# Kernel tuning notes

Hardware: AMD Instinct MI355X
Metric: run time of the kernel (lower is better)

Reference implementation:

```python
import jax, jax.numpy as jnp
import numpy as np
import math

N_QUBITS = 8
N_QLAYERS = 1
LN_EPS = 1e-5


def _rx(state, theta, wire, n):
    # state: (N, 2,...,2) complex64 with n qubit axes; theta: (N,)
    sh = (theta.shape[0],) + (1,) * (n - 1)
    c = jnp.cos(theta / 2).reshape(sh)
    s = jnp.sin(theta / 2).reshape(sh)
    a = jax.lax.index_in_dim(state, 0, wire + 1, keepdims=False)
    b = jax.lax.index_in_dim(state, 1, wire + 1, keepdims=False)
    return jnp.stack([c * a - 1j * s * b, -1j * s * a + c * b], axis=wire + 1)


def _cnot(state, cw, tw, n):
    s0 = jax.lax.index_in_dim(state, 0, cw + 1, keepdims=False)
    s1 = jax.lax.index_in_dim(state, 1, cw + 1, keepdims=False)
    t_ax = tw + 1 if tw < cw else tw  # target axis index after removing control axis
    s1 = jnp.flip(s1, axis=t_ax)
    return jnp.stack([s0, s1], axis=cw + 1)


def _quantum(angles, qweights):
    # AngleEmbedding (RX) + BasicEntanglerLayers (RX + CNOT ring) + PauliZ expvals
    # angles: (N, 8) float; qweights: (1, 8) float -> returns (N, 8) float
    n = N_QUBITS
    N = angles.shape[0]
    state = jnp.zeros((N,) + (2,) * n, jnp.complex64)
    state = state.at[(slice(None),) + (0,) * n].set(1.0 + 0j)
    for w in range(n):
        state = _rx(state, angles[:, w], w, n)
    for l in range(N_QLAYERS):
        for w in range(n):
            state = _rx(state, jnp.broadcast_to(qweights[l, w], (N,)), w, n)
        for cw in range(n):
            state = _cnot(state, cw, (cw + 1) % n, n)
    probs = state.real ** 2 + state.imag ** 2
    zs = []
    for w in range(n):
        p = probs.sum(axis=tuple(a for a in range(1, n + 1) if a != w + 1))  # (N, 2)
        zs.append(p[:, 0] - p[:, 1])
    return jnp.stack(zs, axis=-1)


def _layernorm(x, g, b):
    m = x.mean(-1, keepdims=True)
    v = ((x - m) ** 2).mean(-1, keepdims=True)
    return (x - m) / jnp.sqrt(v + LN_EPS) * g + b


def _forward(x, Wq, Wk, Wv, Wo, ln1_g, ln1_b, W1, b1, W2, b2, ln2_g, ln2_b,
             ql1_w, ql1_b, qweights, ql2_w, ql2_b):
    B, S, D = x.shape
    H = 16
    dk = D // H
    q = (x @ Wq.T).reshape(B, S, H, dk)
    k = (x @ Wk.T).reshape(B, S, H, dk)
    v = (x @ Wv.T).reshape(B, S, H, dk)
    scores = jnp.einsum('bqhd,bkhd->bhqk', q, k) * (1.0 / math.sqrt(dk))
    attn = jax.nn.softmax(scores, axis=-1)
    o = jnp.einsum('bhqk,bkhd->bqhd', attn, v).reshape(B, S, D) @ Wo.T
    x = _layernorm(o + x, ln1_g, ln1_b)
    ff = jax.nn.relu(x @ W1.T + b1) @ W2.T + b2
    x = _layernorm(ff + x, ln2_g, ln2_b)
    angles = (x @ ql1_w.T + ql1_b).reshape(B * S, N_QUBITS)
    z = _quantum(angles, qweights).reshape(B, S, N_QUBITS).astype(x.dtype)
    y = jnp.concatenate([z, x], axis=2) @ ql2_w.T + ql2_b
    return y


def setup_inputs() -> dict:
    key = jax.random.key(0)
    ks = jax.random.split(key, 12)
    B, S, D, F = 4, 1024, 1024, 4096
    sc = 0.02
    w = lambda k, *sh: jax.random.normal(k, sh, jnp.float32) * sc
    return {
        'x': jax.random.normal(ks[0], (B, S, D), jnp.float32),
        'Wq': w(ks[1], D, D), 'Wk': w(ks[2], D, D), 'Wv': w(ks[3], D, D), 'Wo': w(ks[4], D, D),
        'ln1_g': jnp.ones((D,), jnp.float32), 'ln1_b': jnp.zeros((D,), jnp.float32),
        'W1': w(ks[5], F, D), 'b1': jnp.zeros((F,), jnp.float32),
        'W2': w(ks[6], D, F), 'b2': jnp.zeros((D,), jnp.float32),
        'ln2_g': jnp.ones((D,), jnp.float32), 'ln2_b': jnp.zeros((D,), jnp.float32),
        'ql1_w': w(ks[7], N_QUBITS, D), 'ql1_b': jnp.zeros((N_QUBITS,), jnp.float32),
        'qweights': jax.random.uniform(ks[8], (N_QLAYERS, N_QUBITS), jnp.float32, 0.0, 2 * np.pi),
        'ql2_w': w(ks[9], D, D + N_QUBITS), 'ql2_b': jnp.zeros((D,), jnp.float32),
    }


def reference(x, Wq, Wk, Wv, Wo, ln1_g, ln1_b, W1, b1, W2, b2, ln2_g, ln2_b,
              ql1_w, ql1_b, qweights, ql2_w, ql2_b):
    return _forward(x, Wq, Wk, Wv, Wo, ln1_g, ln1_b, W1, b1, W2, b2, ln2_g, ln2_b,
                    ql1_w, ql1_b, qweights, ql2_w, ql2_b)
```

## Files before the change

kernel.cpp:

```cpp
#include <hip/hip_runtime.h>
#include <hip/hip_bf16.h>

typedef __bf16 bf16_t;
typedef __attribute__((ext_vector_type(8))) __bf16 bf16x8;
typedef __attribute__((ext_vector_type(4))) float floatx4;

#define BM 128

enum { EPI_NONE = 0, EPI_RESID, EPI_BIAS_RELU, EPI_BIAS_RESID, EPI_QL2, EPI_PART };

__device__ __forceinline__ void gld_lds16(const bf16_t* g, bf16_t* l) {
  __builtin_amdgcn_global_load_lds(
      (__attribute__((address_space(1))) void*)(g),
      (__attribute__((address_space(3))) void*)(l), 16, 0, 0);
}

template<int ROWS, int COLS>
__device__ __forceinline__ void stage_swz(const bf16_t* g, int ld, bf16_t* lds, int tid) {
  constexpr int G = COLS / 8;
  #pragma unroll
  for (int i = 0; i < ROWS * G / 256; ++i) {
    int ci = i * 256 + tid;
    int row = ci / G, cc = ci % G;
    int gg = (G == 8) ? (cc ^ (row & 7)) : ((cc & 8) | ((cc & 7) ^ (row & 7)));
    gld_lds16(g + (size_t)row * ld + gg * 8, lds + ci * 8);
  }
}

__device__ __forceinline__ int xcd_remap(int id, int nwg) {
  return (id & 7) * (nwg >> 3) + (id >> 3);
}

__device__ __forceinline__ void core128(const bf16_t* __restrict__ Ag,
                                        const bf16_t* __restrict__ Bg,
                                        int Kloop, int lda, int ldb,
                                        bf16_t* As, bf16_t* Bs,
                                        floatx4 acc[4][4]) {
  const int tid = threadIdx.x;
  const int wid = tid >> 6, lane = tid & 63;
  const int wm = (wid >> 1) * 64, wn = (wid & 1) * 64;
  const int m16 = lane & 15, quad = lane >> 4;
  const int r7 = m16 & 7;
  constexpr int BUF = BM * 64;
  stage_swz<128, 64>(Ag, lda, As, tid);
  stage_swz<128, 64>(Bg, ldb, Bs, tid);
  asm volatile("s_waitcnt vmcnt(0)" ::: "memory");
  __syncthreads();
  int cur = 0;
  for (int k0 = 0; k0 < Kloop; k0 += 64) {
    if (k0 + 64 < Kloop) {
      stage_swz<128, 64>(Ag + k0 + 64, lda, As + (cur ^ 1) * BUF, tid);
      stage_swz<128, 64>(Bg + k0 + 64, ldb, Bs + (cur ^ 1) * BUF, tid);
    }
    const bf16_t* Ab = As + cur * BUF;
    const bf16_t* Bb = Bs + cur * BUF;
    #pragma unroll
    for (int ks = 0; ks < 2; ++ks) {
      const int gi = ks * 4 + quad;
      const int slot = gi ^ r7;
      bf16x8 af[4], bfr[4];
      #pragma unroll
      for (int mt = 0; mt < 4; ++mt)
        af[mt] = *(const bf16x8*)&Ab[((wm + mt * 16 + m16) * 8 + slot) * 8];
      #pragma unroll
      for (int nt = 0; nt < 4; ++nt)
        bfr[nt] = *(const bf16x8*)&Bb[((wn + nt * 16 + m16) * 8 + slot) * 8];
      #pragma unroll
      for (int mt = 0; mt < 4; ++mt)
        #pragma unroll
        for (int nt = 0; nt < 4; ++nt)
          acc[mt][nt] = __builtin_amdgcn_mfma_f32_16x16x32_bf16(af[mt], bfr[nt], acc[mt][nt], 0, 0, 0);
    }
    asm volatile("s_waitcnt vmcnt(0)" ::: "memory");
    __syncthreads();
    cur ^= 1;
  }
}

template<int EPI>
__global__ __launch_bounds__(256)
void gemm128(const bf16_t* __restrict__ A, const bf16_t* __restrict__ B,
             bf16_t* __restrict__ C, const float* __restrict__ bias,
             int N, int K, int mblocks, int nblocks) {
  __shared__ bf16_t As[2 * BM * 64];
  __shared__ bf16_t Bs[2 * BM * 64];
  const int tid = threadIdx.x;
  const int wid = tid >> 6, lane = tid & 63;
  const int wm = (wid >> 1) * 64, wn = (wid & 1) * 64;
  const int m16 = lane & 15, quad = lane >> 4;
  const int id = xcd_remap(blockIdx.x, gridDim.x);
  const int per_group = 8 * nblocks;
  const int grp = id / per_group, rem = id % per_group;
  const int m0 = (grp * 8 + (rem & 7)) * BM;
  const int n0 = (rem >> 3) * BM;
  floatx4 acc[4][4];
  const floatx4 vzero = {0.f, 0.f, 0.f, 0.f};
  #pragma unroll
  for (int mt = 0; mt < 4; ++mt)
    #pragma unroll
    for (int nt = 0; nt < 4; ++nt) acc[mt][nt] = vzero;
  core128(A + (size_t)m0 * K, B + (size_t)n0 * K, K, K, K, As, Bs, acc);
  #pragma unroll
  for (int mt = 0; mt < 4; ++mt)
    #pragma unroll
    for (int nt = 0; nt < 4; ++nt) {
      const int gcol = n0 + wn + nt * 16 + m16;
      float bv = (EPI == EPI_BIAS_RELU) ? bias[gcol] : 0.f;
      #pragma unroll
      for (int r = 0; r < 4; ++r) {
        const int grow = m0 + wm + mt * 16 + quad * 4 + r;
        float v = acc[mt][nt][r];
        if (EPI == EPI_BIAS_RELU) { v += bv; v = fmaxf(v, 0.f); }
        C[(size_t)grow * N + gcol] = (bf16_t)v;
      }
    }
}

__global__ __launch_bounds__(256)
void gemm128_sk(const bf16_t* __restrict__ A, const bf16_t* __restrict__ B,
                bf16_t* __restrict__ p0, bf16_t* __restrict__ p1,
                int N, int K, int ldb, int mblocks, int nblocks) {
  __shared__ bf16_t As[2 * BM * 64];
  __shared__ bf16_t Bs[2 * BM * 64];
  const int tid = threadIdx.x;
  const int wid = tid >> 6, lane = tid & 63;
  const int wm = (wid >> 1) * 64, wn = (wid & 1) * 64;
  const int m16 = lane & 15, quad = lane >> 4;
  const int id = xcd_remap(blockIdx.x, gridDim.x);
  const int per_kh = mblocks * nblocks;
  const int kh = id / per_kh;
  const int rem2 = id % per_kh;
  const int per_group = 8 * nblocks;
  const int grp = rem2 / per_group, rem = rem2 % per_group;
  const int m0 = (grp * 8 + (rem & 7)) * BM;
  const int n0 = (rem >> 3) * BM;
  const int Keff = K / 2;
  floatx4 acc[4][4];
  const floatx4 vzero = {0.f, 0.f, 0.f, 0.f};
  #pragma unroll
  for (int mt = 0; mt < 4; ++mt)
    #pragma unroll
    for (int nt = 0; nt < 4; ++nt) acc[mt][nt] = vzero;
  core128(A + (size_t)m0 * K + (size_t)kh * Keff,
          B + (size_t)n0 * ldb + (size_t)kh * Keff, Keff, K, ldb, As, Bs, acc);
  bf16_t* Cp = kh ? p1 : p0;
  #pragma unroll
  for (int mt = 0; mt < 4; ++mt)
    #pragma unroll
    for (int nt = 0; nt < 4; ++nt) {
      const int gcol = n0 + wn + nt * 16 + m16;
      #pragma unroll
      for (int r = 0; r < 4; ++r) {
        const int grow = m0 + wm + mt * 16 + quad * 4 + r;
        Cp[(size_t)grow * N + gcol] = (bf16_t)acc[mt][nt][r];
      }
    }
}

__global__ __launch_bounds__(256)
void gemm_qkv(const bf16_t* __restrict__ X, const bf16_t* __restrict__ Wb,
              bf16_t* __restrict__ Qo, bf16_t* __restrict__ Ko, bf16_t* __restrict__ Vt) {
  __shared__ bf16_t As[2 * BM * 64];
  __shared__ bf16_t Bs[2 * BM * 64];
  const int tid = threadIdx.x;
  const int wid = tid >> 6, lane = tid & 63;
  const int wm = (wid >> 1) * 64, wn = (wid & 1) * 64;
  const int m16 = lane & 15, quad = lane >> 4;
  const int id = xcd_remap(blockIdx.x, gridDim.x);
  const int per_group = 8 * 24;
  const int grp = id / per_group, rem = id % per_group;
  const int m0 = (grp * 8 + (rem & 7)) * BM;
  const int nall = rem >> 3;
  const int n0 = (nall & 7) * BM;
  const int sel = nall >> 3;
  const bf16_t* B = Wb + (size_t)sel * 1024 * 1024;
  floatx4 acc[4][4];
  const floatx4 vzero = {0.f, 0.f, 0.f, 0.f};
  #pragma unroll
  for (int mt = 0; mt < 4; ++mt)
    #pragma unroll
    for (int nt = 0; nt < 4; ++nt) acc[mt][nt] = vzero;
  core128(X + (size_t)m0 * 1024, B + (size_t)n0 * 1024, 1024, 1024, 1024, As, Bs, acc);
  if (sel < 2) {
    bf16_t* C = sel ? Ko : Qo;
    const float sc = sel ? 1.f : 0.125f;
    #pragma unroll
    for (int mt = 0; mt < 4; ++mt)
      #pragma unroll
      for (int nt = 0; nt < 4; ++nt) {
        const int gcol = n0 + wn + nt * 16 + m16;
        #pragma unroll
        for (int r = 0; r < 4; ++r) {
          const int grow = m0 + wm + mt * 16 + quad * 4 + r;
          C[(size_t)grow * 1024 + gcol] = (bf16_t)(acc[mt][nt][r] * sc);
        }
      }
  } else {
    #pragma unroll
    for (int mt = 0; mt < 4; ++mt) {
      const int grow0 = m0 + wm + mt * 16 + quad * 4;
      const int b = grow0 >> 10, s = grow0 & 1023;
      #pragma unroll
      for (int nt = 0; nt < 4; ++nt) {
        const int gcol = n0 + wn + nt * 16 + m16;
        const int h = gcol >> 6, d = gcol & 63;
        #pragma unroll
        for (int r = 0; r < 4; ++r)
          Vt[(((size_t)b * 16 + h) * 64 + d) * 1024 + s + r] = (bf16_t)acc[mt][nt][r];
      }
    }
  }
}

template<int EPI, bool OUTF32>
__global__ __launch_bounds__(256)
void gemm64(const bf16_t* __restrict__ A, const bf16_t* __restrict__ B,
            void* __restrict__ Cv,
            const bf16_t* __restrict__ resid, const float* __restrict__ bias,
            const bf16_t* __restrict__ z, const float* __restrict__ zw,
            int N, int K, int ldb, int boff, int mblocks) {
  __shared__ bf16_t As[BM * 128];
  __shared__ bf16_t Bs[64 * 128];
  const int tid = threadIdx.x;
  const int wid = tid >> 6, lane = tid & 63;
  const int wm = (wid >> 1) * 64, wn = (wid & 1) * 32;
  const int m16 = lane & 15, quad = lane >> 4;
  const int r7 = m16 & 7;
  const int id = xcd_remap(blockIdx.x, gridDim.x);
  const int nb_ = N >> 6;
  const int per_group = 8 * nb_;
  const int grp = id / per_group, rem = id % per_group;
  const int m0 = (grp * 8 + (rem & 7)) * BM;
  const int n0 = (rem >> 3) * 64;
  const bf16_t* Ag = A + (size_t)m0 * K;
  const bf16_t* Bg = B + (size_t)n0 * ldb + boff;
  floatx4 acc[4][2];
  const floatx4 vzero = {0.f, 0.f, 0.f, 0.f};
  #pragma unroll
  for (int mt = 0; mt < 4; ++mt)
    #pragma unroll
    for (int nt = 0; nt < 2; ++nt) acc[mt][nt] = vzero;
  for (int k0 = 0; k0 < K; k0 += 128) {
    stage_swz<128, 128>(Ag + k0, K, As, tid);
    stage_swz<64, 128>(Bg + k0, ldb, Bs, tid);
    __syncthreads();
    #pragma unroll
    for (int ks = 0; ks < 4; ++ks) {
      const int gi = ks * 4 + quad;
      const int slot = (gi & 8) | ((gi & 7) ^ r7);
      bf16x8 af[4], bfr[2];
      #pragma unroll
      for (int mt = 0; mt < 4; ++mt)
        af[mt] = *(const bf16x8*)&As[((wm + mt * 16 + m16) * 16 + slot) * 8];
      #pragma unroll
      for (int nt = 0; nt < 2; ++nt)
        bfr[nt] = *(const bf16x8*)&Bs[((wn + nt * 16 + m16) * 16 + slot) * 8];
      #pragma unroll
      for (int mt = 0; mt < 4; ++mt)
        #pragma unroll
        for (int nt = 0; nt < 2; ++nt)
          acc[mt][nt] = __builtin_amdgcn_mfma_f32_16x16x32_bf16(af[mt], bfr[nt], acc[mt][nt], 0, 0, 0);
    }
    __syncthreads();
  }
  #pragma unroll
  for (int mt = 0; mt < 4; ++mt)
    #pragma unroll
    for (int nt = 0; nt < 2; ++nt) {
      const int gcol = n0 + wn + nt * 16 + m16;
      float bv = 0.f;
      if (EPI == EPI_QL2) bv = bias[gcol];
      #pragma unroll
      for (int r = 0; r < 4; ++r) {
        const int grow = m0 + wm + mt * 16 + quad * 4 + r;
        float v = acc[mt][nt][r];
        if (EPI == EPI_RESID) v += (float)resid[(size_t)grow * N + gcol];
        if (EPI == EPI_QL2) {
          float s = 0.f;
          #pragma unroll
          for (int u = 0; u < 8; ++u)
            s += (float)z[(size_t)grow * 8 + u] * zw[(size_t)gcol * 1032 + u];
          v += bv + s;
        }
        if (OUTF32) ((float*)Cv)[(size_t)grow * N + gcol] = v;
        else        ((bf16_t*)Cv)[(size_t)grow * N + gcol] = (bf16_t)v;
      }
    }
}

__global__ __launch_bounds__(256)
void attn_kernel(const bf16_t* __restrict__ Q, const bf16_t* __restrict__ Kb,
                 const bf16_t* __restrict__ Vt, bf16_t* __restrict__ O) {
  __shared__ bf16_t Qs[64 * 64];
  __shared__ bf16_t Ks[128 * 64];
  __shared__ bf16_t Vs[64 * 128];
  __shared__ bf16_t Ps[4][16 * 128];
  const int tid = threadIdx.x;
  const int wid = tid >> 6, lane = tid & 63;
  const int m16 = lane & 15, quad = lane >> 4;
  const int qt = blockIdx.x, bh = blockIdx.y;
  const int b = bh >> 4, h = bh & 15;
  const size_t qbase = ((size_t)(b * 1024 + qt * 64)) * 1024 + h * 64;
  #pragma unroll
  for (int i = 0; i < 2; ++i) {
    int ci = i * 256 + tid;
    int row = ci >> 3, cc = ci & 7;
    *(bf16x8*)&Qs[row * 64 + ((cc ^ (row & 7)) * 8)] =
        *(const bf16x8*)&Q[qbase + (size_t)row * 1024 + cc * 8];
  }
  __syncthreads();
  const int qm = wid * 16 + m16;
  bf16x8 qf0 = *(const bf16x8*)&Qs[qm * 64 + ((quad ^ (qm & 7)) * 8)];
  bf16x8 qf1 = *(const bf16x8*)&Qs[qm * 64 + (((4 + quad) ^ (qm & 7)) * 8)];
  floatx4 oacc[4];
  float rs[4];
  const floatx4 vzero = {0.f, 0.f, 0.f, 0.f};
  #pragma unroll
  for (int dt = 0; dt < 4; ++dt) oacc[dt] = vzero;
  #pragma unroll
  for (int r = 0; r < 4; ++r) rs[r] = 0.f;
  const size_t kbase = ((size_t)(b * 1024)) * 1024 + h * 64;
  const size_t vbase = ((size_t)bh * 64) * 1024;
  for (int kt = 0; kt < 8; ++kt) {
    __syncthreads();
    #pragma unroll
    for (int i = 0; i < 4; ++i) {
      int ci = i * 256 + tid;
      int row = ci >> 3, cc = ci & 7;
      *(bf16x8*)&Ks[row * 64 + ((cc ^ (row & 7)) * 8)] =
          *(const bf16x8*)&Kb[kbase + (size_t)(kt * 128 + row) * 1024 + cc * 8];
    }
    #pragma unroll
    for (int i = 0; i < 4; ++i) {
      int ci = i * 256 + tid;
      int dr = ci >> 4, cc = ci & 15;
      int gs = (cc & 8) | ((cc & 7) ^ (dr & 7));
      *(bf16x8*)&Vs[dr * 128 + gs * 8] =
          *(const bf16x8*)&Vt[vbase + (size_t)dr * 1024 + kt * 128 + cc * 8];
    }
    __syncthreads();
    floatx4 sa[8];
    #pragma unroll
    for (int nt = 0; nt < 8; ++nt) sa[nt] = vzero;
    #pragma unroll
    for (int nt = 0; nt < 8; ++nt) {
      const int n = nt * 16 + m16;
      bf16x8 kf0 = *(const bf16x8*)&Ks[n * 64 + ((quad ^ (n & 7)) * 8)];
      bf16x8 kf1 = *(const bf16x8*)&Ks[n * 64 + (((4 + quad) ^ (n & 7)) * 8)];
      sa[nt] = __builtin_amdgcn_mfma_f32_16x16x32_bf16(qf0, kf0, sa[nt], 0, 0, 0);
      sa[nt] = __builtin_amdgcn_mfma_f32_16x16x32_bf16(qf1, kf1, sa[nt], 0, 0, 0);
    }
    #pragma unroll
    for (int nt = 0; nt < 8; ++nt)
      #pragma unroll
      for (int r = 0; r < 4; ++r) {
        float pv = __expf(sa[nt][r]);
        rs[r] += pv;
        const int prow = quad * 4 + r;
        const int g = nt * 2 + (m16 >> 3);
        const int gs = (g & 8) | ((g & 7) ^ (prow & 7));
        Ps[wid][prow * 128 + gs * 8 + (m16 & 7)] = (bf16_t)pv;
      }
    bf16x8 pf[4];
    #pragma unroll
    for (int ksub = 0; ksub < 4; ++ksub) {
      const int g = ksub * 4 + quad;
      const int gs = (g & 8) | ((g & 7) ^ (m16 & 7));
      pf[ksub] = *(const bf16x8*)&Ps[wid][m16 * 128 + gs * 8];
    }
    #pragma unroll
    for (int dt = 0; dt < 4; ++dt) {
      const int n = dt * 16 + m16;
      #pragma unroll
      for (int ksub = 0; ksub < 4; ++ksub) {
        const int g = ksub * 4 + quad;
        const int gs = (g & 8) | ((g & 7) ^ (n & 7));
        bf16x8 vf = *(const bf16x8*)&Vs[n * 128 + gs * 8];
        oacc[dt] = __builtin_amdgcn_mfma_f32_16x16x32_bf16(pf[ksub], vf, oacc[dt], 0, 0, 0);
      }
    }
  }
  #pragma unroll
  for (int r = 0; r < 4; ++r) {
    rs[r] += __shfl_xor(rs[r], 1);
    rs[r] += __shfl_xor(rs[r], 2);
    rs[r] += __shfl_xor(rs[r], 4);
    rs[r] += __shfl_xor(rs[r], 8);
  }
  const size_t obase = ((size_t)(b * 1024 + qt * 64 + wid * 16)) * 1024 + h * 64;
  #pragma unroll
  for (int dt = 0; dt < 4; ++dt)
    #pragma unroll
    for (int r = 0; r < 4; ++r)
      O[obase + (size_t)(quad * 4 + r) * 1024 + dt * 16 + m16] = (bf16_t)(oacc[dt][r] / rs[r]);
}

struct Segs {
  const float* s[5];
  bf16_t* d[5];
  int n8[5];
};
__global__ __launch_bounds__(256)
void conv_multi(Segs sg) {
  const int zz = blockIdx.z;
  const float* in = sg.s[zz];
  bf16_t* out = sg.d[zz];
  const int n8 = sg.n8[zz];
  for (int i = blockIdx.x * 256 + threadIdx.x; i < n8; i += gridDim.x * 256) {
    const float* p = in + (size_t)i * 8;
    floatx4 a = *(const floatx4*)p;
    floatx4 b = *(const floatx4*)(p + 4);
    bf16x8 o;
    #pragma unroll
    for (int j = 0; j < 4; ++j) { o[j] = (bf16_t)a[j]; o[4 + j] = (bf16_t)b[j]; }
    *(bf16x8*)(out + (size_t)i * 8) = o;
  }
}

__global__ __launch_bounds__(256)
void ln_combine(const bf16_t* __restrict__ p0, const bf16_t* __restrict__ p1,
                const bf16_t* __restrict__ resid,
                const float* __restrict__ g, const float* __restrict__ b,
                bf16_t* __restrict__ out) {
  const int row = blockIdx.x * 4 + (threadIdx.x >> 6);
  const int lane = threadIdx.x & 63;
  const size_t base = (size_t)row * 1024 + lane * 16;
  bf16x8 a0 = *(const bf16x8*)&p0[base];
  bf16x8 a1 = *(const bf16x8*)&p0[base + 8];
  bf16x8 b0 = *(const bf16x8*)&p1[base];
  bf16x8 b1 = *(const bf16x8*)&p1[base + 8];
  bf16x8 c0 = *(const bf16x8*)&resid[base];
  bf16x8 c1 = *(const bf16x8*)&resid[base + 8];
  float f[16];
  #pragma unroll
  for (int j = 0; j < 8; ++j) {
    f[j]     = (float)a0[j] + (float)b0[j] + (float)c0[j];
    f[8 + j] = (float)a1[j] + (float)b1[j] + (float)c1[j];
  }
  float s = 0.f, ss = 0.f;
  #pragma unroll
  for (int j = 0; j < 16; ++j) { s += f[j]; ss += f[j] * f[j]; }
  #pragma unroll
  for (int off = 1; off < 64; off <<= 1) { s += __shfl_xor(s, off); ss += __shfl_xor(ss, off); }
  const float m = s * (1.f / 1024.f);
  const float inv_sd = rsqrtf(ss * (1.f / 1024.f) - m * m + 1e-5f);
  const float* gp = g + lane * 16;
  const float* bp = b + lane * 16;
  bf16x8 o0, o1;
  #pragma unroll
  for (int j = 0; j < 8; ++j) o0[j] = (bf16_t)((f[j] - m) * inv_sd * gp[j] + bp[j]);
  #pragma unroll
  for (int j = 0; j < 8; ++j) o1[j] = (bf16_t)((f[8 + j] - m) * inv_sd * gp[8 + j] + bp[8 + j]);
  *(bf16x8*)&out[base] = o0;
  *(bf16x8*)&out[base + 8] = o1;
}

__global__ __launch_bounds__(256)
void ln2_quantum(const bf16_t* __restrict__ p0, const bf16_t* __restrict__ p1,
                 const bf16_t* __restrict__ resid, const float* __restrict__ bias,
                 const float* __restrict__ g, const float* __restrict__ b,
                 bf16_t* __restrict__ x2,
                 const float* __restrict__ qw1, const float* __restrict__ qb1,
                 const float* __restrict__ qwt, bf16_t* __restrict__ zout,
                 const float* __restrict__ ql2w, bf16_t* __restrict__ ql2wb) {
  if (blockIdx.z == 1) {
    const int n8 = 1024 * 1032 / 8;
    for (int i = blockIdx.x * 256 + threadIdx.x; i < n8; i += gridDim.x * 256) {
      const float* p = ql2w + (size_t)i * 8;
      floatx4 a = *(const floatx4*)p;
      floatx4 bb = *(const floatx4*)(p + 4);
      bf16x8 o;
      #pragma unroll
      for (int j = 0; j < 4; ++j) { o[j] = (bf16_t)a[j]; o[4 + j] = (bf16_t)bb[j]; }
      *(bf16x8*)(ql2wb + (size_t)i * 8) = o;
    }
    return;
  }
  const int row = blockIdx.x * 4 + (threadIdx.x >> 6);
  const int lane = threadIdx.x & 63;
  const size_t base = (size_t)row * 1024 + lane * 16;
  bf16x8 a0 = *(const bf16x8*)&p0[base];
  bf16x8 a1 = *(const bf16x8*)&p0[base + 8];
  bf16x8 b0 = *(const bf16x8*)&p1[base];
  bf16x8 b1 = *(const bf16x8*)&p1[base + 8];
  bf16x8 c0 = *(const bf16x8*)&resid[base];
  bf16x8 c1 = *(const bf16x8*)&resid[base + 8];
  const float* bsp = bias + lane * 16;
  float f[16];
  #pragma unroll
  for (int j = 0; j < 8; ++j) {
    f[j]     = (float)a0[j] + (float)b0[j] + (float)c0[j] + bsp[j];
    f[8 + j] = (float)a1[j] + (float)b1[j] + (float)c1[j] + bsp[8 + j];
  }
  float s = 0.f, ss = 0.f;
  #pragma unroll
  for (int j = 0; j < 16; ++j) { s += f[j]; ss += f[j] * f[j]; }
  #pragma unroll
  for (int off = 1; off < 64; off <<= 1) { s += __shfl_xor(s, off); ss += __shfl_xor(ss, off); }
  const float m = s * (1.f / 1024.f);
  const float inv_sd = rsqrtf(ss * (1.f / 1024.f) - m * m + 1e-5f);
  const float* gp = g + lane * 16;
  const float* bp = b + lane * 16;
  bf16x8 o0, o1;
  #pragma unroll
  for (int j = 0; j < 8; ++j) o0[j] = (bf16_t)((f[j] - m) * inv_sd * gp[j] + bp[j]);
  #pragma unroll
  for (int j = 0; j < 8; ++j) o1[j] = (bf16_t)((f[8 + j] - m) * inv_sd * gp[8 + j] + bp[8 + j]);
  *(bf16x8*)&x2[base] = o0;
  *(bf16x8*)&x2[base + 8] = o1;
  float th[8];
  #pragma unroll
  for (int qq = 0; qq < 8; ++qq) {
    const float* wp = qw1 + (size_t)qq * 1024 + lane * 16;
    float sdot = 0.f;
    #pragma unroll
    for (int j = 0; j < 8; ++j)
      sdot += (float)o0[j] * wp[j] + (float)o1[j] * wp[8 + j];
    #pragma unroll
    for (int off = 1; off < 64; off <<= 1) sdot += __shfl_xor(sdot, off);
    th[qq] = sdot + qb1[qq] + qwt[qq];
  }
  if (lane == 0) {
    float c[8];
    #pragma unroll
    for (int qq = 0; qq < 8; ++qq) c[qq] = cosf(th[qq]);
    float z0 = 1.f;
    #pragma unroll
    for (int u = 1; u < 8; ++u) z0 *= c[u];
    zout[(size_t)row * 8 + 0] = (bf16_t)z0;
    float pp = c[0];
    #pragma unroll
    for (int w = 1; w < 8; ++w) { pp *= c[w]; zout[(size_t)row * 8 + w] = (bf16_t)pp; }
  }
}

extern "C" void kernel_launch(void* const* d_in, const int* in_sizes, int n_in,
                              void* d_out, int out_size, void* d_ws, size_t ws_size,
                              hipStream_t stream) {
  const float* x    = (const float*)d_in[0];
  const float* Wq   = (const float*)d_in[1];
  const float* Wk   = (const float*)d_in[2];
  const float* Wv   = (const float*)d_in[3];
  const float* Wo   = (const float*)d_in[4];
  const float* ln1g = (const float*)d_in[5];
  const float* ln1b = (const float*)d_in[6];
  const float* W1   = (const float*)d_in[7];
  const float* b1   = (const float*)d_in[8];
  const float* W2   = (const float*)d_in[9];
  const float* b2   = (const float*)d_in[10];
  const float* ln2g = (const float*)d_in[11];
  const float* ln2b = (const float*)d_in[12];
  const float* qw1  = (const float*)d_in[13];
  const float* qb1  = (const float*)d_in[14];
  const float* qwt  = (const float*)d_in[15];
  const float* ql2w = (const float*)d_in[16];
  const float* ql2b = (const float*)d_in[17];
  bf16_t* ws = (bf16_t*)d_ws;

  const size_t T = (size_t)4096 * 1024;
  const size_t M1 = (size_t)1024 * 1024;
  bf16_t* outlo = (bf16_t*)d_out;
  bf16_t* outhi = outlo + T;

  bf16_t* xb    = ws;
  bf16_t* kb    = ws + T;
  bf16_t* vt    = ws + 2 * T;
  bf16_t* ff    = ws + 3 * T;
  bf16_t* wqkvb = ff;
  bf16_t* wob   = ff + 3 * M1;
  bf16_t* w1b   = vt;
  bf16_t* w2b   = kb;
  bf16_t* ql2wb = ff;
  bf16_t* q     = outlo;
  bf16_t* o     = outhi;
  bf16_t* x1    = outhi;
  bf16_t* x2    = vt;
  bf16_t* z     = kb;

  {
    Segs sg;
    sg.s[0] = x;  sg.d[0] = xb;            sg.n8[0] = (int)(T / 8);
    sg.s[1] = Wq; sg.d[1] = wqkvb;         sg.n8[1] = (int)(M1 / 8);
    sg.s[2] = Wk; sg.d[2] = wqkvb + M1;    sg.n8[2] = (int)(M1 / 8);
    sg.s[3] = Wv; sg.d[3] = wqkvb + 2*M1;  sg.n8[3] = (int)(M1 / 8);
    sg.s[4] = Wo; sg.d[4] = wob;           sg.n8[4] = (int)(M1 / 8);
    conv_multi<<<dim3(512, 1, 5), 256, 0, stream>>>(sg);
  }
  gemm_qkv<<<768, 256, 0, stream>>>(xb, wqkvb, q, kb, vt);
  attn_kernel<<<dim3(16, 64), 256, 0, stream>>>(q, kb, vt, o);
  gemm128_sk<<<512, 256, 0, stream>>>(o, wob, outlo, kb, 1024, 1024, 1024, 32, 8);
  ln_combine<<<1024, 256, 0, stream>>>(outlo, kb, xb, ln1g, ln1b, x1);
  {
    Segs sg;
    sg.s[0] = W1; sg.d[0] = w1b; sg.n8[0] = (int)(T / 8);
    sg.s[1] = W2; sg.d[1] = w2b; sg.n8[1] = (int)(T / 8);
    sg.s[2] = nullptr; sg.d[2] = nullptr; sg.n8[2] = 0;
    sg.s[3] = nullptr; sg.d[3] = nullptr; sg.n8[3] = 0;
    sg.s[4] = nullptr; sg.d[4] = nullptr; sg.n8[4] = 0;
    conv_multi<<<dim3(1024, 1, 2), 256, 0, stream>>>(sg);
  }
  gemm128<EPI_BIAS_RELU><<<1024, 256, 0, stream>>>(x1, w1b, ff, b1, 4096, 1024, 32, 32);
  gemm128_sk<<<512, 256, 0, stream>>>(ff, w2b, xb, vt, 1024, 4096, 4096, 32, 8);
  ln2_quantum<<<dim3(1024, 1, 2), 256, 0, stream>>>(
      xb, vt, x1, b2, ln2g, ln2b, x2, qw1, qb1, qwt, z, ql2w, ql2wb);
  gemm64<EPI_QL2, true><<<512, 256, 0, stream>>>(
      x2, ql2wb, d_out, nullptr, ql2b, z, ql2w, 1024, 1024, 1032, 8, 32);
}
```

Before: 384.1 us.

## Double-buffer K tiles with async LDS loads and remap attention grid

Rewrites the attention kernel's staging to use direct global-to-LDS async loads (stage_swz). K tiles are double-buffered so the next tile's load overlaps the QK^T MFMA and softmax of the current one, and the V tile load overlaps the score computation. The grid is flattened to 1D and remapped so neighbouring blocks spread across batch-heads, which is meant to change L2/XCD locality. The kernel uses more LDS for the second K buffer and adds an extra barrier per iteration, which may reduce occupancy.

```diff
diff --git a/kernel.cpp b/kernel.cpp
--- a/kernel.cpp
+++ b/kernel.cpp
@@ -292,15 +292,19 @@
 void attn_kernel(const bf16_t* __restrict__ Q, const bf16_t* __restrict__ Kb,
                  const bf16_t* __restrict__ Vt, bf16_t* __restrict__ O) {
   __shared__ bf16_t Qs[64 * 64];
-  __shared__ bf16_t Ks[128 * 64];
+  __shared__ bf16_t Ks[2][128 * 64];
   __shared__ bf16_t Vs[64 * 128];
   __shared__ bf16_t Ps[4][16 * 128];
   const int tid = threadIdx.x;
   const int wid = tid >> 6, lane = tid & 63;
   const int m16 = lane & 15, quad = lane >> 4;
-  const int qt = blockIdx.x, bh = blockIdx.y;
+  const int id = blockIdx.x;
+  const int bh = (id & 7) * 8 + ((id >> 3) & 7);
+  const int qt = id >> 6;
   const int b = bh >> 4, h = bh & 15;
   const size_t qbase = ((size_t)(b * 1024 + qt * 64)) * 1024 + h * 64;
+  const size_t kbase = ((size_t)(b * 1024)) * 1024 + h * 64;
+  const size_t vbase = ((size_t)bh * 64) * 1024;
   #pragma unroll
   for (int i = 0; i < 2; ++i) {
     int ci = i * 256 + tid;
@@ -308,6 +312,8 @@
     *(bf16x8*)&Qs[row * 64 + ((cc ^ (row & 7)) * 8)] =
         *(const bf16x8*)&Q[qbase + (size_t)row * 1024 + cc * 8];
   }
+  stage_swz<128, 64>(Kb + kbase, 1024, Ks[0], tid);
+  asm volatile("s_waitcnt vmcnt(0)" ::: "memory");
   __syncthreads();
   const int qm = wid * 16 + m16;
   bf16x8 qf0 = *(const bf16x8*)&Qs[qm * 64 + ((quad ^ (qm & 7)) * 8)];
@@ -319,34 +325,19 @@
   for (int dt = 0; dt < 4; ++dt) oacc[dt] = vzero;
   #pragma unroll
   for (int r = 0; r < 4; ++r) rs[r] = 0.f;
-  const size_t kbase = ((size_t)(b * 1024)) * 1024 + h * 64;
-  const size_t vbase = ((size_t)bh * 64) * 1024;
   for (int kt = 0; kt < 8; ++kt) {
-    __syncthreads();
-    #pragma unroll
-    for (int i = 0; i < 4; ++i) {
-      int ci = i * 256 + tid;
-      int row = ci >> 3, cc = ci & 7;
-      *(bf16x8*)&Ks[row * 64 + ((cc ^ (row & 7)) * 8)] =
-          *(const bf16x8*)&Kb[kbase + (size_t)(kt * 128 + row) * 1024 + cc * 8];
-    }
-    #pragma unroll
-    for (int i = 0; i < 4; ++i) {
-      int ci = i * 256 + tid;
-      int dr = ci >> 4, cc = ci & 15;
-      int gs = (cc & 8) | ((cc & 7) ^ (dr & 7));
-      *(bf16x8*)&Vs[dr * 128 + gs * 8] =
-          *(const bf16x8*)&Vt[vbase + (size_t)dr * 1024 + kt * 128 + cc * 8];
-    }
-    __syncthreads();
+    stage_swz<64, 128>(Vt + vbase + kt * 128, 1024, Vs, tid);
+    if (kt < 7)
+      stage_swz<128, 64>(Kb + kbase + (size_t)(kt + 1) * 128 * 1024, 1024, Ks[(kt + 1) & 1], tid);
+    const bf16_t* Kc = Ks[kt & 1];
     floatx4 sa[8];
     #pragma unroll
     for (int nt = 0; nt < 8; ++nt) sa[nt] = vzero;
     #pragma unroll
     for (int nt = 0; nt < 8; ++nt) {
       const int n = nt * 16 + m16;
-      bf16x8 kf0 = *(const bf16x8*)&Ks[n * 64 + ((quad ^ (n & 7)) * 8)];
-      bf16x8 kf1 = *(const bf16x8*)&Ks[n * 64 + (((4 + quad) ^ (n & 7)) * 8)];
+      bf16x8 kf0 = *(const bf16x8*)&Kc[n * 64 + ((quad ^ (n & 7)) * 8)];
+      bf16x8 kf1 = *(const bf16x8*)&Kc[n * 64 + (((4 + quad) ^ (n & 7)) * 8)];
       sa[nt] = __builtin_amdgcn_mfma_f32_16x16x32_bf16(qf0, kf0, sa[nt], 0, 0, 0);
       sa[nt] = __builtin_amdgcn_mfma_f32_16x16x32_bf16(qf1, kf1, sa[nt], 0, 0, 0);
     }
@@ -361,6 +352,8 @@
         const int gs = (g & 8) | ((g & 7) ^ (prow & 7));
         Ps[wid][prow * 128 + gs * 8 + (m16 & 7)] = (bf16_t)pv;
       }
+    asm volatile("s_waitcnt vmcnt(0)" ::: "memory");
+    __syncthreads();
     bf16x8 pf[4];
     #pragma unroll
     for (int ksub = 0; ksub < 4; ++ksub) {
@@ -379,6 +372,7 @@
         oacc[dt] = __builtin_amdgcn_mfma_f32_16x16x32_bf16(pf[ksub], vf, oacc[dt], 0, 0, 0);
       }
     }
+    __syncthreads();
   }
   #pragma unroll
   for (int r = 0; r < 4; ++r) {
@@ -587,7 +581,7 @@
     conv_multi<<<dim3(512, 1, 5), 256, 0, stream>>>(sg);
   }
   gemm_qkv<<<768, 256, 0, stream>>>(xb, wqkvb, q, kb, vt);
-  attn_kernel<<<dim3(16, 64), 256, 0, stream>>>(q, kb, vt, o);
+  attn_kernel<<<1024, 256, 0, stream>>>(q, kb, vt, o);
   gemm128_sk<<<512, 256, 0, stream>>>(o, wob, outlo, kb, 1024, 1024, 1024, 32, 8);
   ln_combine<<<1024, 256, 0, stream>>>(outlo, kb, xb, ln1g, ln1b, x1);
   {
```

Measured after the change: 376.3 us. 2.1% less time.
